# Kernel tuning notes

Measured on AMD Instinct MI355X. Metric: run time of the kernel, lower is better.

## Reference

```python
import jax, jax.numpy as jnp
import numpy as np

N = 100000      # nodes
E = 1600000     # directed edges (avg degree 16)
D_IN, D_H, D_OUT = 128, 128, 64


def glorot(k, fi, fo):
    s = (6.0 / (fi + fo)) ** 0.5
    return jax.random.uniform(k, (fi, fo), jnp.float32, -s, s)


def setup_inputs() -> dict:
    key = jax.random.key(0)
    ks = jax.random.split(key, 5)
    edges = jax.random.randint(ks[0], (2, E), 0, N)
    features = jax.random.normal(ks[1], (N, D_IN), dtype=jnp.float32)
    return dict(
        edges=edges,
        features=features,
        W0=glorot(ks[2], D_IN, D_H), b0=jnp.zeros((D_H,), jnp.float32),
        W1=glorot(ks[3], D_H, D_H), b1=jnp.zeros((D_H,), jnp.float32),
        W2=glorot(ks[4], D_H, D_OUT), b2=jnp.zeros((D_OUT,), jnp.float32),
    )


def _prep(edges):
    # add self-loops and compute symmetric GCN normalization D^-1/2 A_hat D^-1/2
    loop = jnp.arange(N)
    row = jnp.concatenate([edges[0], loop])  # source
    col = jnp.concatenate([edges[1], loop])  # target
    deg = jax.ops.segment_sum(jnp.ones((row.shape[0],), jnp.float32), col, num_segments=N)
    dinv = jnp.where(deg > 0, jax.lax.rsqrt(deg), 0.0)
    norm = dinv[row] * dinv[col]             # per-edge coefficient
    return row, col, norm


def gcn_conv(x, row, col, norm, W, b):
    x = x @ W                                 # [N, out]
    msg = x[row] * norm[:, None]              # gather + scale, [E+N, out]
    return jax.ops.segment_sum(msg, col, num_segments=N) + b


def reference(edges, features, W0, b0, W1, b1, W2, b2):
    row, col, norm = _prep(edges)
    h = jax.nn.relu(gcn_conv(features, row, col, norm, W0, b0))
    h = jax.nn.relu(gcn_conv(h, row, col, norm, W1, b1))
    h = gcn_conv(h, row, col, norm, W2, b2)
    return jax.nn.log_softmax(h, axis=1)
```

## Files before the change

kernel.cpp:

```cpp
#include <hip/hip_runtime.h>
#include <hip/hip_fp16.h>
#include <math.h>

#define NN 100000
#define EE 1600000
#define NB2 782
#define BN 128
#define NPART 512
#define CAP 2560

typedef __attribute__((ext_vector_type(8))) _Float16 half8;
typedef __attribute__((ext_vector_type(4))) float f32x4;
typedef __attribute__((ext_vector_type(4))) unsigned int u32x4;

__device__ inline unsigned short f2h(float x) {
    return __half_as_ushort(__float2half(x));
}
__device__ inline __half2 u2h2(unsigned u) {
    return __builtin_bit_cast(__half2, u);
}
__device__ inline unsigned h22u(__half2 h) {
    return __builtin_bit_cast(unsigned, h);
}


__global__ void prep_weights(const float* __restrict__ W0, const float* __restrict__ W1,
                             const float* __restrict__ W2, unsigned short* __restrict__ Wt0,
                             unsigned short* __restrict__ Wt1, unsigned short* __restrict__ Wt2,
                             int* __restrict__ bcount) {
    int g = blockIdx.x * 256 + threadIdx.x;
    if (g < NB2) bcount[g] = 0;
    if (g < 16384) {
        int n = g >> 7, k = g & 127;
        Wt0[g] = f2h(W0[k * 128 + n]);
    } else if (g < 32768) {
        int i = g - 16384;
        int n = i >> 7, k = i & 127;
        Wt1[i] = f2h(W1[k * 128 + n]);
    } else if (g < 40960) {
        int i = g - 32768;
        int n = i >> 7, k = i & 127;
        Wt2[i] = f2h(W2[k * 64 + n]);
    }
}


__global__ __launch_bounds__(256) void scatter_bump(const int* __restrict__ src,
                                                    const int* __restrict__ dst,
                                                    int* __restrict__ bcount,
                                                    int* __restrict__ P, int e) {
    __shared__ int cnt[NB2];
    __shared__ int basep[NB2];
    __shared__ int cur[NB2];
    int t = threadIdx.x;
    for (int i = t; i < NB2; i += 256) { cnt[i] = 0; cur[i] = 0; }
    __syncthreads();
    int chunk = (e + NPART - 1) / NPART;
    int b0 = blockIdx.x * chunk, b1 = min(e, b0 + chunk);
    for (int i = b0 + t; i < b1; i += 256)
        atomicAdd(&cnt[dst[i] >> 7], 1);
    __syncthreads();
    for (int i = t; i < NB2; i += 256) {
        int c = cnt[i];
        basep[i] = c ? atomicAdd(&bcount[i], c) : 0;
    }
    __syncthreads();
    for (int i = b0 + t; i < b1; i += 256) {
        int d = dst[i];
        int b = d >> 7;
        int p = basep[b] + atomicAdd(&cur[b], 1);
        P[(size_t)b * CAP + p] = (src[i] << 7) | (d & 127);
    }
}

__global__ __launch_bounds__(256) void bucket_build(const int* __restrict__ P,
                                                    const int* __restrict__ bcount,
                                                    int2* __restrict__ offs2,
                                                    float* __restrict__ dinv,
                                                    int* __restrict__ csr, int n) {
    __shared__ int cnt[BN];
    __shared__ int sc[BN];
    __shared__ int cur[BN];
    __shared__ int stage[CAP];
    int b = blockIdx.x, t = threadIdx.x;
    int base = b * CAP;
    int count = bcount[b];
    if (t < BN) cnt[t] = 0;
    __syncthreads();
    for (int i = t; i < count; i += 256)
        atomicAdd(&cnt[P[base + i] & 127], 1);
    __syncthreads();
    int v = 0;
    if (t < BN) {
        v = cnt[t];
        sc[t] = v;
    }
    for (int d = 1; d < BN; d <<= 1) {
        __syncthreads();
        int x = (t < BN && t >= d) ? sc[t - d] : 0;
        __syncthreads();
        if (t < BN) sc[t] += x;
    }
    __syncthreads();
    if (t < BN) {
        int myoff = sc[t] - v;
        int node = b * BN + t;
        if (node < n) {
            offs2[node] = make_int2(base + myoff, base + myoff + v);
            dinv[node] = 1.0f / sqrtf((float)(v + 1));
        }
        cur[t] = myoff;
    }
    __syncthreads();
    for (int i = t; i < count; i += 256) {
        int pe = P[base + i];
        int p = atomicAdd(&cur[pe & 127], 1);
        stage[p] = ((unsigned)pe) >> 7;
    }
    __syncthreads();
    for (int i = t; i < count; i += 256) csr[base + i] = stage[i];
}

template <bool F32>
__device__ inline half8 load_xrow(const void* A, int row, int col, int nrows) {
    if (row >= nrows) {
        u32x4 z = {0u, 0u, 0u, 0u};
        return __builtin_bit_cast(half8, z);
    }
    if (F32) {
        const float* p = (const float*)A + (size_t)row * 128 + col;
        float4 v0 = *(const float4*)p;
        float4 v1 = *(const float4*)(p + 4);
        u32x4 u;
        u.x = h22u(__floats2half2_rn(v0.x, v0.y));
        u.y = h22u(__floats2half2_rn(v0.z, v0.w));
        u.z = h22u(__floats2half2_rn(v1.x, v1.y));
        u.w = h22u(__floats2half2_rn(v1.z, v1.w));
        return __builtin_bit_cast(half8, u);
    } else {
        const unsigned short* p = (const unsigned short*)A + (size_t)row * 128 + col;
        u32x4 u = *(const u32x4*)p;
        return __builtin_bit_cast(half8, u);
    }
}

template <int DOUT, bool A_IS_F32>
__global__ __launch_bounds__(256) void gemm_mfma(const void* __restrict__ Aptr,
                                                 const unsigned short* __restrict__ Wt,
                                                 const float* __restrict__ dinv,
                                                 unsigned short* __restrict__ Y, int nrows) {
    constexpr int KP = 136;
    constexpr int NT = DOUT / 16;
    __shared__ unsigned short sB[DOUT * KP];
    const int row0 = blockIdx.x * 128;
    const int tid = threadIdx.x;

    for (int i = tid; i < DOUT * 16; i += 256) {
        int n = i >> 4, c = (i & 15) * 8;
        uint4 v = *(const uint4*)(Wt + n * 128 + c);
        *(uint4*)(&sB[n * KP + c]) = v;
    }
    __syncthreads();

    const int wave = tid >> 6;
    const int lane = tid & 63;
    const int m0 = lane & 15;
    const int kq = (lane >> 4) * 8;
    const int xr0 = row0 + wave * 32 + m0;
    const int xr1 = xr0 + 16;

    f32x4 acc[2][NT];
#pragma unroll
    for (int rt = 0; rt < 2; ++rt)
#pragma unroll
        for (int t = 0; t < NT; ++t) acc[rt][t] = (f32x4){0.f, 0.f, 0.f, 0.f};

#pragma unroll
    for (int k0 = 0; k0 < 128; k0 += 32) {
        half8 b0 = load_xrow<A_IS_F32>(Aptr, xr0, k0 + kq, nrows);
        half8 b1 = load_xrow<A_IS_F32>(Aptr, xr1, k0 + kq, nrows);
#pragma unroll
        for (int t = 0; t < NT; ++t) {
            half8 aW = *(const half8*)(&sB[(t * 16 + m0) * KP + k0 + kq]);
            acc[0][t] = __builtin_amdgcn_mfma_f32_16x16x32_f16(aW, b0, acc[0][t], 0, 0, 0);
            acc[1][t] = __builtin_amdgcn_mfma_f32_16x16x32_f16(aW, b1, acc[1][t], 0, 0, 0);
        }
    }

#pragma unroll
    for (int rt = 0; rt < 2; ++rt) {
        int xrow = row0 + wave * 32 + rt * 16 + m0;
        if (xrow < nrows) {
            float dv = dinv[xrow];
#pragma unroll
            for (int t = 0; t < NT; ++t) {
                uint2 o;
                o.x = h22u(__floats2half2_rn(acc[rt][t][0] * dv, acc[rt][t][1] * dv));
                o.y = h22u(__floats2half2_rn(acc[rt][t][2] * dv, acc[rt][t][3] * dv));
                *(uint2*)(Y + (size_t)xrow * DOUT + t * 16 + (lane >> 4) * 4) = o;
            }
        }
    }
}

__global__ __launch_bounds__(256) void agg128_f16(const unsigned short* __restrict__ Xp,
                                                  const int* __restrict__ csr,
                                                  const int2* __restrict__ offs2,
                                                  const float* __restrict__ dinv,
                                                  const float* __restrict__ bias,
                                                  unsigned short* __restrict__ Y, int n) {
    const int tid = threadIdx.x;
    const int node = blockIdx.x * 16 + (tid >> 4);
    if (node >= n) return;
    const int l = tid & 15;
    const unsigned short* __restrict__ Xl = Xp + l * 8;

    int2 se = offs2[node];
    int s = se.x, deg = se.y - se.x;
    const __half2 hz = __floats2half2_rn(0.f, 0.f);
    __half2 aA0 = hz, aA1 = hz, aA2 = hz, aA3 = hz;
    __half2 aB0 = hz, aB1 = hz, aB2 = hz, aB3 = hz;
    int j = 0;
    for (; j + 4 <= deg; j += 4) {
        int i0 = csr[s + j], i1 = csr[s + j + 1], i2 = csr[s + j + 2], i3 = csr[s + j + 3];
        uint4 u0 = *(const uint4*)(Xl + (size_t)i0 * 128);
        uint4 u1 = *(const uint4*)(Xl + (size_t)i1 * 128);
        uint4 u2 = *(const uint4*)(Xl + (size_t)i2 * 128);
        uint4 u3 = *(const uint4*)(Xl + (size_t)i3 * 128);
        aA0 = __hadd2(aA0, u2h2(u0.x)); aA1 = __hadd2(aA1, u2h2(u0.y));
        aA2 = __hadd2(aA2, u2h2(u0.z)); aA3 = __hadd2(aA3, u2h2(u0.w));
        aB0 = __hadd2(aB0, u2h2(u2.x)); aB1 = __hadd2(aB1, u2h2(u2.y));
        aB2 = __hadd2(aB2, u2h2(u2.z)); aB3 = __hadd2(aB3, u2h2(u2.w));
        aA0 = __hadd2(aA0, u2h2(u1.x)); aA1 = __hadd2(aA1, u2h2(u1.y));
        aA2 = __hadd2(aA2, u2h2(u1.z)); aA3 = __hadd2(aA3, u2h2(u1.w));
        aB0 = __hadd2(aB0, u2h2(u3.x)); aB1 = __hadd2(aB1, u2h2(u3.y));
        aB2 = __hadd2(aB2, u2h2(u3.z)); aB3 = __hadd2(aB3, u2h2(u3.w));
    }
    for (; j < deg; ++j) {
        int i0 = csr[s + j];
        uint4 u = *(const uint4*)(Xl + (size_t)i0 * 128);
        aA0 = __hadd2(aA0, u2h2(u.x)); aA1 = __hadd2(aA1, u2h2(u.y));
        aA2 = __hadd2(aA2, u2h2(u.z)); aA3 = __hadd2(aA3, u2h2(u.w));
    }
    {
        uint4 u = *(const uint4*)(Xl + (size_t)node * 128);
        aB0 = __hadd2(aB0, u2h2(u.x)); aB1 = __hadd2(aB1, u2h2(u.y));
        aB2 = __hadd2(aB2, u2h2(u.z)); aB3 = __hadd2(aB3, u2h2(u.w));
    }
    float di = dinv[node];
    float4 bA = *(const float4*)(bias + l * 8);
    float4 bB = *(const float4*)(bias + l * 8 + 4);
    float2 fA, fB;
    fA = __half22float2(aA0); fB = __half22float2(aB0);
    float r0 = fA.x + fB.x, r1 = fA.y + fB.y;
    fA = __half22float2(aA1); fB = __half22float2(aB1);
    float r2 = fA.x + fB.x, r3 = fA.y + fB.y;
    fA = __half22float2(aA2); fB = __half22float2(aB2);
    float r4 = fA.x + fB.x, r5 = fA.y + fB.y;
    fA = __half22float2(aA3); fB = __half22float2(aB3);
    float r6 = fA.x + fB.x, r7 = fA.y + fB.y;
    r0 = fmaxf(fmaf(di, r0, bA.x), 0.f); r1 = fmaxf(fmaf(di, r1, bA.y), 0.f);
    r2 = fmaxf(fmaf(di, r2, bA.z), 0.f); r3 = fmaxf(fmaf(di, r3, bA.w), 0.f);
    r4 = fmaxf(fmaf(di, r4, bB.x), 0.f); r5 = fmaxf(fmaf(di, r5, bB.y), 0.f);
    r6 = fmaxf(fmaf(di, r6, bB.z), 0.f); r7 = fmaxf(fmaf(di, r7, bB.w), 0.f);
    uint4 o;
    o.x = h22u(__floats2half2_rn(r0, r1));
    o.y = h22u(__floats2half2_rn(r2, r3));
    o.z = h22u(__floats2half2_rn(r4, r5));
    o.w = h22u(__floats2half2_rn(r6, r7));
    *(uint4*)(Y + (size_t)node * 128 + l * 8) = o;
}

__global__ __launch_bounds__(256) void agg_softmax64_f16(const unsigned short* __restrict__ Xp,
                                                         const int* __restrict__ csr,
                                                         const int2* __restrict__ offs2,
                                                         const float* __restrict__ dinv,
                                                         const float* __restrict__ bias,
                                                         float* __restrict__ out, int n) {
    __shared__ int sIdx[4][64];
    int wv = threadIdx.x >> 6;
    int node = blockIdx.x * 4 + wv;
    if (node >= n) return;
    int lane = threadIdx.x & 63;
    int g8 = lane >> 3;
    int l = lane & 7;
    int2 se = offs2[node];
    int s = se.x, deg = se.y - se.x;
    if (lane < deg) sIdx[wv][lane] = csr[s + lane];
    int dcap = min(deg, 64);
    const int* idx = sIdx[wv];
    const __half2 hz = __floats2half2_rn(0.f, 0.f);
    __half2 aA0 = hz, aA1 = hz, aA2 = hz, aA3 = hz;
    __half2 aB0 = hz, aB1 = hz, aB2 = hz, aB3 = hz;
    int j = g8;
    for (; j + 8 < dcap; j += 16) {
        int s0 = idx[j], s1 = idx[j + 8];
        uint4 u0 = *(const uint4*)(Xp + (size_t)s0 * 64 + l * 8);
        uint4 u1 = *(const uint4*)(Xp + (size_t)s1 * 64 + l * 8);
        aA0 = __hadd2(aA0, u2h2(u0.x)); aA1 = __hadd2(aA1, u2h2(u0.y));
        aA2 = __hadd2(aA2, u2h2(u0.z)); aA3 = __hadd2(aA3, u2h2(u0.w));
        aB0 = __hadd2(aB0, u2h2(u1.x)); aB1 = __hadd2(aB1, u2h2(u1.y));
        aB2 = __hadd2(aB2, u2h2(u1.z)); aB3 = __hadd2(aB3, u2h2(u1.w));
    }
    if (j < dcap) {
        int s0 = idx[j];
        uint4 u = *(const uint4*)(Xp + (size_t)s0 * 64 + l * 8);
        aA0 = __hadd2(aA0, u2h2(u.x)); aA1 = __hadd2(aA1, u2h2(u.y));
        aA2 = __hadd2(aA2, u2h2(u.z)); aA3 = __hadd2(aA3, u2h2(u.w));
    }
    for (int p = s + 64 + g8; p < s + deg; p += 8) {
        int s0 = csr[p];
        uint4 u = *(const uint4*)(Xp + (size_t)s0 * 64 + l * 8);
        aB0 = __hadd2(aB0, u2h2(u.x)); aB1 = __hadd2(aB1, u2h2(u.y));
        aB2 = __hadd2(aB2, u2h2(u.z)); aB3 = __hadd2(aB3, u2h2(u.w));
    }
    if (g8 == 0) {
        uint4 u = *(const uint4*)(Xp + (size_t)node * 64 + l * 8);
        aB0 = __hadd2(aB0, u2h2(u.x)); aB1 = __hadd2(aB1, u2h2(u.y));
        aB2 = __hadd2(aB2, u2h2(u.z)); aB3 = __hadd2(aB3, u2h2(u.w));
    }
    float2 fA, fB;
    fA = __half22float2(aA0); fB = __half22float2(aB0);
    float r0 = fA.x + fB.x, r1 = fA.y + fB.y;
    fA = __half22float2(aA1); fB = __half22float2(aB1);
    float r2 = fA.x + fB.x, r3 = fA.y + fB.y;
    fA = __half22float2(aA2); fB = __half22float2(aB2);
    float r4 = fA.x + fB.x, r5 = fA.y + fB.y;
    fA = __half22float2(aA3); fB = __half22float2(aB3);
    float r6 = fA.x + fB.x, r7 = fA.y + fB.y;
    r0 += __shfl_xor(r0, 8); r0 += __shfl_xor(r0, 16); r0 += __shfl_xor(r0, 32);
    r1 += __shfl_xor(r1, 8); r1 += __shfl_xor(r1, 16); r1 += __shfl_xor(r1, 32);
    r2 += __shfl_xor(r2, 8); r2 += __shfl_xor(r2, 16); r2 += __shfl_xor(r2, 32);
    r3 += __shfl_xor(r3, 8); r3 += __shfl_xor(r3, 16); r3 += __shfl_xor(r3, 32);
    r4 += __shfl_xor(r4, 8); r4 += __shfl_xor(r4, 16); r4 += __shfl_xor(r4, 32);
    r5 += __shfl_xor(r5, 8); r5 += __shfl_xor(r5, 16); r5 += __shfl_xor(r5, 32);
    r6 += __shfl_xor(r6, 8); r6 += __shfl_xor(r6, 16); r6 += __shfl_xor(r6, 32);
    r7 += __shfl_xor(r7, 8); r7 += __shfl_xor(r7, 16); r7 += __shfl_xor(r7, 32);
    if (g8 == 0) {
        float di = dinv[node];
        float4 bA = *(const float4*)(bias + l * 8);
        float4 bB = *(const float4*)(bias + l * 8 + 4);
        r0 = fmaf(di, r0, bA.x); r1 = fmaf(di, r1, bA.y);
        r2 = fmaf(di, r2, bA.z); r3 = fmaf(di, r3, bA.w);
        r4 = fmaf(di, r4, bB.x); r5 = fmaf(di, r5, bB.y);
        r6 = fmaf(di, r6, bB.z); r7 = fmaf(di, r7, bB.w);
        float m = fmaxf(fmaxf(fmaxf(r0, r1), fmaxf(r2, r3)), fmaxf(fmaxf(r4, r5), fmaxf(r6, r7)));
#pragma unroll
        for (int o = 4; o > 0; o >>= 1) m = fmaxf(m, __shfl_xor(m, o));
        float ssum = __expf(r0 - m) + __expf(r1 - m) + __expf(r2 - m) + __expf(r3 - m) +
                     __expf(r4 - m) + __expf(r5 - m) + __expf(r6 - m) + __expf(r7 - m);
#pragma unroll
        for (int o = 4; o > 0; o >>= 1) ssum += __shfl_xor(ssum, o);
        float lg = m + __logf(ssum);
        float4 o0 = make_float4(r0 - lg, r1 - lg, r2 - lg, r3 - lg);
        float4 o1 = make_float4(r4 - lg, r5 - lg, r6 - lg, r7 - lg);
        *(float4*)(out + (size_t)node * 64 + l * 8) = o0;
        *(float4*)(out + (size_t)node * 64 + l * 8 + 4) = o1;
    }
}


extern "C" void kernel_launch(void* const* d_in, const int* in_sizes, int n_in,
                              void* d_out, int out_size, void* d_ws, size_t ws_size,
                              hipStream_t stream) {
    const int* edges = (const int*)d_in[0];
    const float* feat = (const float*)d_in[1];
    const float* W0 = (const float*)d_in[2];
    const float* b0 = (const float*)d_in[3];
    const float* W1 = (const float*)d_in[4];
    const float* b1 = (const float*)d_in[5];
    const float* W2 = (const float*)d_in[6];
    const float* b2 = (const float*)d_in[7];

    const int N = NN;
    const int E = EE;

    char* ws = (char*)d_ws;
    int* bcount = (int*)ws;
    int2* offs2 = (int2*)(bcount + ((NB2 + 1) & ~1));
    float* dinv = (float*)(offs2 + N);
    int* P = (int*)(dinv + N);
    int* csr = P + (size_t)NB2 * CAP;
    unsigned short* Wt0 = (unsigned short*)(csr + (size_t)NB2 * CAP);
    unsigned short* Wt1 = Wt0 + 16384;
    unsigned short* Wt2 = Wt1 + 16384;
    size_t off = (size_t)((char*)(Wt2 + 8192) - ws);
    off = (off + 255) & ~(size_t)255;
    unsigned short* bufA = (unsigned short*)(ws + off);
    unsigned short* bufB = bufA + (size_t)N * 128;

    const int* esrc = edges;
    const int* edst = edges + E;

    prep_weights<<<160, 256, 0, stream>>>(W0, W1, W2, Wt0, Wt1, Wt2, bcount);
    scatter_bump<<<NPART, 256, 0, stream>>>(esrc, edst, bcount, P, E);
    bucket_build<<<NB2, 256, 0, stream>>>(P, bcount, offs2, dinv, csr, N);

    const int gemmBlocks = (N + 127) / 128;
    const int agg128Blocks = (N + 15) / 16;
    const int aggBlocks = (N + 3) / 4;

    gemm_mfma<128, true><<<gemmBlocks, 256, 0, stream>>>(feat, Wt0, dinv, bufA, N);
    agg128_f16<<<agg128Blocks, 256, 0, stream>>>(bufA, csr, offs2, dinv, b0, bufB, N);
    gemm_mfma<128, false><<<gemmBlocks, 256, 0, stream>>>(bufB, Wt1, dinv, bufA, N);
    agg128_f16<<<agg128Blocks, 256, 0, stream>>>(bufA, csr, offs2, dinv, b1, bufB, N);
    gemm_mfma<64, false><<<gemmBlocks, 256, 0, stream>>>(bufB, Wt2, dinv, bufA, N);
    agg_softmax64_f16<<<aggBlocks, 256, 0, stream>>>(bufA, csr, offs2, dinv, b2, (float*)d_out, N);
}
```

Measured before the change: 369.3 us.

## Fold weight prep into scatter, unroll agg128 by 8, remap softmax agg to 8 lanes/node

Moves the weight transpose/convert into the scatter_bump kernel and replaces the bcount zeroing with a memset, saving one kernel launch. Adds an 8-way unrolled gather loop to agg128 for more loads in flight. Rewrites the final softmax aggregation so each node uses 8 lanes with a sequential 8-way unrolled gather instead of a 64-lane wave with LDS indices and cross-lane shuffle reductions. This cuts shuffle work and raises node parallelism, at the cost of more per-thread serial work for high-degree nodes.

Result: faster. 351.9 us (median of 2 runs) (-4.7%).

```diff
diff --git a/kernel.cpp b/kernel.cpp
--- a/kernel.cpp
+++ b/kernel.cpp
@@ -24,35 +24,35 @@
 }
 
 
-__global__ void prep_weights(const float* __restrict__ W0, const float* __restrict__ W1,
-                             const float* __restrict__ W2, unsigned short* __restrict__ Wt0,
-                             unsigned short* __restrict__ Wt1, unsigned short* __restrict__ Wt2,
-                             int* __restrict__ bcount) {
-    int g = blockIdx.x * 256 + threadIdx.x;
-    if (g < NB2) bcount[g] = 0;
-    if (g < 16384) {
-        int n = g >> 7, k = g & 127;
-        Wt0[g] = f2h(W0[k * 128 + n]);
-    } else if (g < 32768) {
-        int i = g - 16384;
-        int n = i >> 7, k = i & 127;
-        Wt1[i] = f2h(W1[k * 128 + n]);
-    } else if (g < 40960) {
-        int i = g - 32768;
-        int n = i >> 7, k = i & 127;
-        Wt2[i] = f2h(W2[k * 64 + n]);
-    }
-}
-
-
 __global__ __launch_bounds__(256) void scatter_bump(const int* __restrict__ src,
                                                     const int* __restrict__ dst,
                                                     int* __restrict__ bcount,
-                                                    int* __restrict__ P, int e) {
+                                                    int* __restrict__ P, int e,
+                                                    const float* __restrict__ W0,
+                                                    const float* __restrict__ W1,
+                                                    const float* __restrict__ W2,
+                                                    unsigned short* __restrict__ Wt0,
+                                                    unsigned short* __restrict__ Wt1,
+                                                    unsigned short* __restrict__ Wt2) {
     __shared__ int cnt[NB2];
     __shared__ int basep[NB2];
     __shared__ int cur[NB2];
     int t = threadIdx.x;
+    {
+        int g = blockIdx.x * 256 + t;
+        if (g < 16384) {
+            int n = g >> 7, k = g & 127;
+            Wt0[g] = f2h(W0[k * 128 + n]);
+        } else if (g < 32768) {
+            int i = g - 16384;
+            int n = i >> 7, k = i & 127;
+            Wt1[i] = f2h(W1[k * 128 + n]);
+        } else if (g < 40960) {
+            int i = g - 32768;
+            int n = i >> 7, k = i & 127;
+            Wt2[i] = f2h(W2[k * 64 + n]);
+        }
+    }
     for (int i = t; i < NB2; i += 256) { cnt[i] = 0; cur[i] = 0; }
     __syncthreads();
     int chunk = (e + NPART - 1) / NPART;
@@ -221,6 +221,34 @@
     __half2 aA0 = hz, aA1 = hz, aA2 = hz, aA3 = hz;
     __half2 aB0 = hz, aB1 = hz, aB2 = hz, aB3 = hz;
     int j = 0;
+    for (; j + 8 <= deg; j += 8) {
+        int i0 = csr[s + j],     i1 = csr[s + j + 1], i2 = csr[s + j + 2], i3 = csr[s + j + 3];
+        int i4 = csr[s + j + 4], i5 = csr[s + j + 5], i6 = csr[s + j + 6], i7 = csr[s + j + 7];
+        uint4 u0 = *(const uint4*)(Xl + (size_t)i0 * 128);
+        uint4 u1 = *(const uint4*)(Xl + (size_t)i1 * 128);
+        uint4 u2 = *(const uint4*)(Xl + (size_t)i2 * 128);
+        uint4 u3 = *(const uint4*)(Xl + (size_t)i3 * 128);
+        uint4 u4 = *(const uint4*)(Xl + (size_t)i4 * 128);
+        uint4 u5 = *(const uint4*)(Xl + (size_t)i5 * 128);
+        uint4 u6 = *(const uint4*)(Xl + (size_t)i6 * 128);
+        uint4 u7 = *(const uint4*)(Xl + (size_t)i7 * 128);
+        aA0 = __hadd2(aA0, u2h2(u0.x)); aA1 = __hadd2(aA1, u2h2(u0.y));
+        aA2 = __hadd2(aA2, u2h2(u0.z)); aA3 = __hadd2(aA3, u2h2(u0.w));
+        aB0 = __hadd2(aB0, u2h2(u1.x)); aB1 = __hadd2(aB1, u2h2(u1.y));
+        aB2 = __hadd2(aB2, u2h2(u1.z)); aB3 = __hadd2(aB3, u2h2(u1.w));
+        aA0 = __hadd2(aA0, u2h2(u2.x)); aA1 = __hadd2(aA1, u2h2(u2.y));
+        aA2 = __hadd2(aA2, u2h2(u2.z)); aA3 = __hadd2(aA3, u2h2(u2.w));
+        aB0 = __hadd2(aB0, u2h2(u3.x)); aB1 = __hadd2(aB1, u2h2(u3.y));
+        aB2 = __hadd2(aB2, u2h2(u3.z)); aB3 = __hadd2(aB3, u2h2(u3.w));
+        aA0 = __hadd2(aA0, u2h2(u4.x)); aA1 = __hadd2(aA1, u2h2(u4.y));
+        aA2 = __hadd2(aA2, u2h2(u4.z)); aA3 = __hadd2(aA3, u2h2(u4.w));
+        aB0 = __hadd2(aB0, u2h2(u5.x)); aB1 = __hadd2(aB1, u2h2(u5.y));
+        aB2 = __hadd2(aB2, u2h2(u5.z)); aB3 = __hadd2(aB3, u2h2(u5.w));
+        aA0 = __hadd2(aA0, u2h2(u6.x)); aA1 = __hadd2(aA1, u2h2(u6.y));
+        aA2 = __hadd2(aA2, u2h2(u6.z)); aA3 = __hadd2(aA3, u2h2(u6.w));
+        aB0 = __hadd2(aB0, u2h2(u7.x)); aB1 = __hadd2(aB1, u2h2(u7.y));
+        aB2 = __hadd2(aB2, u2h2(u7.z)); aB3 = __hadd2(aB3, u2h2(u7.w));
+    }
     for (; j + 4 <= deg; j += 4) {
         int i0 = csr[s + j], i1 = csr[s + j + 1], i2 = csr[s + j + 2], i3 = csr[s + j + 3];
         uint4 u0 = *(const uint4*)(Xl + (size_t)i0 * 128);
@@ -229,10 +257,10 @@
         uint4 u3 = *(const uint4*)(Xl + (size_t)i3 * 128);
         aA0 = __hadd2(aA0, u2h2(u0.x)); aA1 = __hadd2(aA1, u2h2(u0.y));
         aA2 = __hadd2(aA2, u2h2(u0.z)); aA3 = __hadd2(aA3, u2h2(u0.w));
-        aB0 = __hadd2(aB0, u2h2(u2.x)); aB1 = __hadd2(aB1, u2h2(u2.y));
-        aB2 = __hadd2(aB2, u2h2(u2.z)); aB3 = __hadd2(aB3, u2h2(u2.w));
-        aA0 = __hadd2(aA0, u2h2(u1.x)); aA1 = __hadd2(aA1, u2h2(u1.y));
-        aA2 = __hadd2(aA2, u2h2(u1.z)); aA3 = __hadd2(aA3, u2h2(u1.w));
+        aB0 = __hadd2(aB0, u2h2(u1.x)); aB1 = __hadd2(aB1, u2h2(u1.y));
+        aB2 = __hadd2(aB2, u2h2(u1.z)); aB3 = __hadd2(aB3, u2h2(u1.w));
+        aA0 = __hadd2(aA0, u2h2(u2.x)); aA1 = __hadd2(aA1, u2h2(u2.y));
+        aA2 = __hadd2(aA2, u2h2(u2.z)); aA3 = __hadd2(aA3, u2h2(u2.w));
         aB0 = __hadd2(aB0, u2h2(u3.x)); aB1 = __hadd2(aB1, u2h2(u3.y));
         aB2 = __hadd2(aB2, u2h2(u3.z)); aB3 = __hadd2(aB3, u2h2(u3.w));
     }
@@ -277,48 +305,60 @@
                                                          const float* __restrict__ dinv,
                                                          const float* __restrict__ bias,
                                                          float* __restrict__ out, int n) {
-    __shared__ int sIdx[4][64];
-    int wv = threadIdx.x >> 6;
-    int node = blockIdx.x * 4 + wv;
+    const int tid = threadIdx.x;
+    const int node = blockIdx.x * 32 + (tid >> 3);
     if (node >= n) return;
-    int lane = threadIdx.x & 63;
-    int g8 = lane >> 3;
-    int l = lane & 7;
+    const int l = tid & 7;
+    const unsigned short* __restrict__ Xl = Xp + l * 8;
+
     int2 se = offs2[node];
     int s = se.x, deg = se.y - se.x;
-    if (lane < deg) sIdx[wv][lane] = csr[s + lane];
-    int dcap = min(deg, 64);
-    const int* idx = sIdx[wv];
     const __half2 hz = __floats2half2_rn(0.f, 0.f);
     __half2 aA0 = hz, aA1 = hz, aA2 = hz, aA3 = hz;
     __half2 aB0 = hz, aB1 = hz, aB2 = hz, aB3 = hz;
-    int j = g8;
-    for (; j + 8 < dcap; j += 16) {
-        int s0 = idx[j], s1 = idx[j + 8];
-        uint4 u0 = *(const uint4*)(Xp + (size_t)s0 * 64 + l * 8);
-        uint4 u1 = *(const uint4*)(Xp + (size_t)s1 * 64 + l * 8);
+    int j = 0;
+    for (; j + 8 <= deg; j += 8) {
+        int i0 = csr[s + j],     i1 = csr[s + j + 1], i2 = csr[s + j + 2], i3 = csr[s + j + 3];
+        int i4 = csr[s + j + 4], i5 = csr[s + j + 5], i6 = csr[s + j + 6], i7 = csr[s + j + 7];
+        uint4 u0 = *(const uint4*)(Xl + (size_t)i0 * 64);
+        uint4 u1 = *(const uint4*)(Xl + (size_t)i1 * 64);
+        uint4 u2 = *(const uint4*)(Xl + (size_t)i2 * 64);
+        uint4 u3 = *(const uint4*)(Xl + (size_t)i3 * 64);
+        uint4 u4 = *(const uint4*)(Xl + (size_t)i4 * 64);
+        uint4 u5 = *(const uint4*)(Xl + (size_t)i5 * 64);
+        uint4 u6 = *(const uint4*)(Xl + (size_t)i6 * 64);
+        uint4 u7 = *(const uint4*)(Xl + (size_t)i7 * 64);
         aA0 = __hadd2(aA0, u2h2(u0.x)); aA1 = __hadd2(aA1, u2h2(u0.y));
         aA2 = __hadd2(aA2, u2h2(u0.z)); aA3 = __hadd2(aA3, u2h2(u0.w));
         aB0 = __hadd2(aB0, u2h2(u1.x)); aB1 = __hadd2(aB1, u2h2(u1.y));
         aB2 = __hadd2(aB2, u2h2(u1.z)); aB3 = __hadd2(aB3, u2h2(u1.w));
-    }
-    if (j < dcap) {
-        int s0 = idx[j];
-        uint4 u = *(const uint4*)(Xp + (size_t)s0 * 64 + l * 8);
+        aA0 = __hadd2(aA0, u2h2(u2.x)); aA1 = __hadd2(aA1, u2h2(u2.y));
+        aA2 = __hadd2(aA2, u2h2(u2.z)); aA3 = __hadd2(aA3, u2h2(u2.w));
+        aB0 = __hadd2(aB0, u2h2(u3.x)); aB1 = __hadd2(aB1, u2h2(u3.y));
+        aB2 = __hadd2(aB2, u2h2(u3.z)); aB3 = __hadd2(aB3, u2h2(u3.w));
+        aA0 = __hadd2(aA0, u2h2(u4.x)); aA1 = __hadd2(aA1, u2h2(u4.y));
+        aA2 = __hadd2(aA2, u2h2(u4.z)); aA3 = __hadd2(aA3, u2h2(u4.w));
+        aB0 = __hadd2(aB0, u2h2(u5.x)); aB1 = __hadd2(aB1, u2h2(u5.y));
+        aB2 = __hadd2(aB2, u2h2(u5.z)); aB3 = __hadd2(aB3, u2h2(u5.w));
+        aA0 = __hadd2(aA0, u2h2(u6.x)); aA1 = __hadd2(aA1, u2h2(u6.y));
+        aA2 = __hadd2(aA2, u2h2(u6.z)); aA3 = __hadd2(aA3, u2h2(u6.w));
+        aB0 = __hadd2(aB0, u2h2(u7.x)); aB1 = __hadd2(aB1, u2h2(u7.y));
+        aB2 = __hadd2(aB2, u2h2(u7.z)); aB3 = __hadd2(aB3, u2h2(u7.w));
+    }
+    for (; j < deg; ++j) {
+        int i0 = csr[s + j];
+        uint4 u = *(const uint4*)(Xl + (size_t)i0 * 64);
         aA0 = __hadd2(aA0, u2h2(u.x)); aA1 = __hadd2(aA1, u2h2(u.y));
         aA2 = __hadd2(aA2, u2h2(u.z)); aA3 = __hadd2(aA3, u2h2(u.w));
     }
-    for (int p = s + 64 + g8; p < s + deg; p += 8) {
-        int s0 = csr[p];
-        uint4 u = *(const uint4*)(Xp + (size_t)s0 * 64 + l * 8);
+    {
+        uint4 u = *(const uint4*)(Xl + (size_t)node * 64);
         aB0 = __hadd2(aB0, u2h2(u.x)); aB1 = __hadd2(aB1, u2h2(u.y));
         aB2 = __hadd2(aB2, u2h2(u.z)); aB3 = __hadd2(aB3, u2h2(u.w));
     }
-    if (g8 == 0) {
-        uint4 u = *(const uint4*)(Xp + (size_t)node * 64 + l * 8);
-        aB0 = __hadd2(aB0, u2h2(u.x)); aB1 = __hadd2(aB1, u2h2(u.y));
-        aB2 = __hadd2(aB2, u2h2(u.z)); aB3 = __hadd2(aB3, u2h2(u.w));
-    }
+    float di = dinv[node];
+    float4 bA = *(const float4*)(bias + l * 8);
+    float4 bB = *(const float4*)(bias + l * 8 + 4);
     float2 fA, fB;
     fA = __half22float2(aA0); fB = __half22float2(aB0);
     float r0 = fA.x + fB.x, r1 = fA.y + fB.y;
@@ -328,35 +368,24 @@
     float r4 = fA.x + fB.x, r5 = fA.y + fB.y;
     fA = __half22float2(aA3); fB = __half22float2(aB3);
     float r6 = fA.x + fB.x, r7 = fA.y + fB.y;
-    r0 += __shfl_xor(r0, 8); r0 += __shfl_xor(r0, 16); r0 += __shfl_xor(r0, 32);
-    r1 += __shfl_xor(r1, 8); r1 += __shfl_xor(r1, 16); r1 += __shfl_xor(r1, 32);
-    r2 += __shfl_xor(r2, 8); r2 += __shfl_xor(r2, 16); r2 += __shfl_xor(r2, 32);
-    r3 += __shfl_xor(r3, 8); r3 += __shfl_xor(r3, 16); r3 += __shfl_xor(r3, 32);
-    r4 += __shfl_xor(r4, 8); r4 += __shfl_xor(r4, 16); r4 += __shfl_xor(r4, 32);
-    r5 += __shfl_xor(r5, 8); r5 += __shfl_xor(r5, 16); r5 += __shfl_xor(r5, 32);
-    r6 += __shfl_xor(r6, 8); r6 += __shfl_xor(r6, 16); r6 += __shfl_xor(r6, 32);
-    r7 += __shfl_xor(r7, 8); r7 += __shfl_xor(r7, 16); r7 += __shfl_xor(r7, 32);
-    if (g8 == 0) {
-        float di = dinv[node];
-        float4 bA = *(const float4*)(bias + l * 8);
-        float4 bB = *(const float4*)(bias + l * 8 + 4);
-        r0 = fmaf(di, r0, bA.x); r1 = fmaf(di, r1, bA.y);
-        r2 = fmaf(di, r2, bA.z); r3 = fmaf(di, r3, bA.w);
-        r4 = fmaf(di, r4, bB.x); r5 = fmaf(di, r5, bB.y);
-        r6 = fmaf(di, r6, bB.z); r7 = fmaf(di, r7, bB.w);
-        float m = fmaxf(fmaxf(fmaxf(r0, r1), fmaxf(r2, r3)), fmaxf(fmaxf(r4, r5), fmaxf(r6, r7)));
-#pragma unroll
-        for (int o = 4; o > 0; o >>= 1) m = fmaxf(m, __shfl_xor(m, o));
-        float ssum = __expf(r0 - m) + __expf(r1 - m) + __expf(r2 - m) + __expf(r3 - m) +
-                     __expf(r4 - m) + __expf(r5 - m) + __expf(r6 - m) + __expf(r7 - m);
-#pragma unroll
-        for (int o = 4; o > 0; o >>= 1) ssum += __shfl_xor(ssum, o);
-        float lg = m + __logf(ssum);
-        float4 o0 = make_float4(r0 - lg, r1 - lg, r2 - lg, r3 - lg);
-        float4 o1 = make_float4(r4 - lg, r5 - lg, r6 - lg, r7 - lg);
-        *(float4*)(out + (size_t)node * 64 + l * 8) = o0;
-        *(float4*)(out + (size_t)node * 64 + l * 8 + 4) = o1;
-    }
+    r0 = fmaf(di, r0, bA.x); r1 = fmaf(di, r1, bA.y);
+    r2 = fmaf(di, r2, bA.z); r3 = fmaf(di, r3, bA.w);
+    r4 = fmaf(di, r4, bB.x); r5 = fmaf(di, r5, bB.y);
+    r6 = fmaf(di, r6, bB.z); r7 = fmaf(di, r7, bB.w);
+    float m = fmaxf(fmaxf(fmaxf(r0, r1), fmaxf(r2, r3)), fmaxf(fmaxf(r4, r5), fmaxf(r6, r7)));
+    m = fmaxf(m, __shfl_xor(m, 1));
+    m = fmaxf(m, __shfl_xor(m, 2));
+    m = fmaxf(m, __shfl_xor(m, 4));
+    float ssum = __expf(r0 - m) + __expf(r1 - m) + __expf(r2 - m) + __expf(r3 - m) +
+                 __expf(r4 - m) + __expf(r5 - m) + __expf(r6 - m) + __expf(r7 - m);
+    ssum += __shfl_xor(ssum, 1);
+    ssum += __shfl_xor(ssum, 2);
+    ssum += __shfl_xor(ssum, 4);
+    float lg = m + __logf(ssum);
+    float4 o0 = make_float4(r0 - lg, r1 - lg, r2 - lg, r3 - lg);
+    float4 o1 = make_float4(r4 - lg, r5 - lg, r6 - lg, r7 - lg);
+    *(float4*)(out + (size_t)node * 64 + l * 8) = o0;
+    *(float4*)(out + (size_t)node * 64 + l * 8 + 4) = o1;
 }
 
 
@@ -392,18 +421,19 @@
     const int* esrc = edges;
     const int* edst = edges + E;
 
-    prep_weights<<<160, 256, 0, stream>>>(W0, W1, W2, Wt0, Wt1, Wt2, bcount);
-    scatter_bump<<<NPART, 256, 0, stream>>>(esrc, edst, bcount, P, E);
+    hipMemsetAsync(bcount, 0, NB2 * sizeof(int), stream);
+    scatter_bump<<<NPART, 256, 0, stream>>>(esrc, edst, bcount, P, E,
+                                            W0, W1, W2, Wt0, Wt1, Wt2);
     bucket_build<<<NB2, 256, 0, stream>>>(P, bcount, offs2, dinv, csr, N);
 
     const int gemmBlocks = (N + 127) / 128;
     const int agg128Blocks = (N + 15) / 16;
-    const int aggBlocks = (N + 3) / 4;
+    const int aggsmBlocks = (N + 31) / 32;
 
     gemm_mfma<128, true><<<gemmBlocks, 256, 0, stream>>>(feat, Wt0, dinv, bufA, N);
     agg128_f16<<<agg128Blocks, 256, 0, stream>>>(bufA, csr, offs2, dinv, b0, bufB, N);
     gemm_mfma<128, false><<<gemmBlocks, 256, 0, stream>>>(bufB, Wt1, dinv, bufA, N);
     agg128_f16<<<agg128Blocks, 256, 0, stream>>>(bufA, csr, offs2, dinv, b1, bufB, N);
     gemm_mfma<64, false><<<gemmBlocks, 256, 0, stream>>>(bufB, Wt2, dinv, bufA, N);
-    agg_softmax64_f16<<<aggBlocks, 256, 0, stream>>>(bufA, csr, offs2, dinv, b2, (float*)d_out, N);
-}
+    agg_softmax64_f16<<<aggsmBlocks, 256, 0, stream>>>(bufA, csr, offs2, dinv, b2, (float*)d_out, N);
+}
```
